# Performance work log

Hardware: AMD Instinct MI355X
Metric: run time of the kernel (lower is better)

## Reference

```python
import jax, jax.numpy as jnp
import numpy as np

B, C, H, W = 8, 64, 128, 128
NH, OPH = 4, 16
MX, MY = 32, 17  # n_modes=(32,32) -> modes_y = 32//2+1
NPAT_S, NPAT_F = 10000, 5000
ED_S, ED_F = 64, 32


def setup_inputs() -> dict:
    ks = jax.random.split(jax.random.key(0), 16)
    n = lambda k, s, sc=1.0: jax.random.normal(k, s, dtype=jnp.float32) * sc
    z = lambda s: jnp.zeros(s, jnp.float32)
    return dict(
        x=n(ks[0], (B, C, H, W)),
        se_emb=n(ks[1], (NPAT_S, ED_S)),
        se_w=n(ks[2], (ED_S, C), 0.1), se_b=z(C),
        mhf_wr=n(ks[3], (NH, C, OPH, MX, MY), 0.01),
        mhf_wi=n(ks[4], (NH, C, OPH, MX, MY), 0.01),
        mhf_bias=z(C),
        sp_emb=n(ks[5], (NPAT_F, ED_F)),
        sp_wr=n(ks[6], (ED_F, C * MX * MY), 0.05), sp_br=z(C * MX * MY),
        sp_wi=n(ks[7], (ED_F, C * MX * MY), 0.05), sp_bi=z(C * MX * MY),
        gate_w1=n(ks[8], (3 * C, 64), 0.05), gate_b1=z(64),
        gate_w2=n(ks[9], (64, 3), 0.05), gate_b2=z(3),
        skip_w=n(ks[10], (C, C), 0.05), skip_b=z(C),
        norm_g=jnp.ones(C), norm_b=z(C),
        mlp_w1=n(ks[11], (C, 2 * C), 0.05), mlp_b1=z(2 * C),
        mlp_w2=n(ks[12], (2 * C, C), 0.05), mlp_b2=z(C),
    )


def _gelu(v):
    return jax.nn.gelu(v, approximate=False)


def _block(x, se_emb, se_w, se_b, mhf_wr, mhf_wi, mhf_bias, sp_emb, sp_wr, sp_br,
           sp_wi, sp_bi, gate_w1, gate_b1, gate_w2, gate_b2, skip_w, skip_b,
           norm_g, norm_b, mlp_w1, mlp_b1, mlp_w2, mlp_b2):
    Bq, Cq, Hq, Wq = x.shape
    # --- SpatialEngram: quantization is elementwise, so sum over window entries
    # equals 3x3 box-sum of the quantized padded field (identical integers,
    # avoids materializing the (B,C,H,W,3,3) unfold tensor).
    xp = jnp.pad(x, ((0, 0), (0, 0), (1, 1), (1, 1)), mode='edge')
    q = (xp * 100.0).astype(jnp.int32)  # trunc toward zero, same as torch .long()
    hv = jnp.zeros((Bq, Cq, Hq, Wq), jnp.int32)
    for i in range(3):
        for j in range(3):
            hv = hv + q[:, :, i:i + Hq, j:j + Wq]
    idx = (jnp.abs(hv) % NPAT_S).astype(jnp.float32).mean(axis=1).astype(jnp.int32)  # (B,H,W)
    spatial = jnp.moveaxis(se_emb[idx] @ se_w + se_b, -1, 1)  # (B,C,H,W)
    # --- MHF multi-head spectral conv (all heads in one einsum; concat == reshape)
    xf = jnp.fft.rfft2(x, norm='ortho')          # (B,C,H,W//2+1) complex64
    lo = xf[:, :, :MX, :MY]
    wc = (mhf_wr + 1j * mhf_wi).astype(lo.dtype)
    of = jnp.einsum('biXY,hioXY->bhoXY', lo, wc).reshape(Bq, Cq, MX, MY)
    full = jnp.zeros((Bq, Cq, Hq, Wq // 2 + 1), lo.dtype).at[:, :, :MX, :MY].set(of)
    mhf = jnp.fft.irfft2(full, s=(Hq, Wq), norm='ortho') + mhf_bias[:, None, None]
    # --- SpectralEngram: per-sample hash of low-freq magnitude -> embedding -> freq proj
    mag = jnp.abs(lo).mean(axis=(1, 2, 3))                       # (B,)
    fidx = (mag * 1000.0).astype(jnp.int32) % NPAT_F
    fe = sp_emb[fidx]                                            # (B,ED_F)
    re = (fe @ sp_wr + sp_br).reshape(Bq, Cq, MX, MY)
    im = (fe @ sp_wi + sp_bi).reshape(Bq, Cq, MX, MY)
    full2 = jnp.zeros((Bq, Cq, Hq, Wq // 2 + 1), lo.dtype).at[:, :, :MX, :MY].set(re + 1j * im)
    spec = jnp.fft.irfft2(full2, s=(Hq, Wq), norm='ortho')
    # --- gated fusion
    gate_in = jnp.concatenate([spatial.mean((2, 3)), mhf.mean((2, 3)), spec.mean((2, 3))], axis=-1)
    gw = jax.nn.softmax(_gelu(gate_in @ gate_w1 + gate_b1) @ gate_w2 + gate_b2, axis=-1)
    a = gw[:, 0, None, None, None]
    bt = gw[:, 1, None, None, None]
    gm = gw[:, 2, None, None, None]
    fused = a * spatial + bt * mhf + gm * spec
    y = fused + jnp.einsum('bihw,io->bohw', x, skip_w) + skip_b[:, None, None]
    # --- GroupNorm(1,C) + 1x1-conv channel MLP (dropout=0)
    mu = y.mean((1, 2, 3), keepdims=True)
    var = y.var((1, 2, 3), keepdims=True)
    yn = (y - mu) * jax.lax.rsqrt(var + 1e-5) * norm_g[:, None, None] + norm_b[:, None, None]
    h = _gelu(jnp.einsum('bihw,io->bohw', yn, mlp_w1) + mlp_b1[:, None, None])
    h = jnp.einsum('bihw,io->bohw', h, mlp_w2) + mlp_b2[:, None, None]
    return y + h


def reference(x, se_emb, se_w, se_b, mhf_wr, mhf_wi, mhf_bias, sp_emb, sp_wr, sp_br,
              sp_wi, sp_bi, gate_w1, gate_b1, gate_w2, gate_b2, skip_w, skip_b,
              norm_g, norm_b, mlp_w1, mlp_b1, mlp_w2, mlp_b2):
    return _block(x, se_emb, se_w, se_b, mhf_wr, mhf_wi, mhf_bias, sp_emb, sp_wr, sp_br,
                  sp_wi, sp_bi, gate_w1, gate_b1, gate_w2, gate_b2, skip_w, skip_b,
                  norm_g, norm_b, mlp_w1, mlp_b1, mlp_w2, mlp_b2)
```

## Files before the change

kernel.cpp:

```cpp
#include <hip/hip_runtime.h>
#include <hip/hip_bf16.h>
#include <math.h>

#define B_ 8
#define C_ 64
#define H_ 128
#define W_ 128
#define NH_ 4
#define OPH_ 16
#define MX_ 32
#define MY_ 17
#define NPAT_F 5000
#define ED_F 32
#define XY_ (MX_*MY_)
#define HW_ (H_*W_)
#define NE_ (B_*C_*H_*W_)

#define OFF_LO     0u
#define OFF_T1     2228224u
#define OFF_T2     2228224u
#define OFF_FMHF   11141120u
#define OFF_FSPEC  13369344u
#define OFF_IDX    33030144u

typedef __hip_bfloat16 bf16;

template<typename T>
__device__ __forceinline__ float ldt(const void* p, int i){ return (float)(((const T*)p)[i]); }

template<typename T>
__device__ __forceinline__ float2 ld2(const void* p, int i){
  if(sizeof(T)==4) return *(const float2*)((const float*)p + i);
  unsigned raw = *(const unsigned*)((const unsigned short*)p + i);
  return make_float2(__uint_as_float(raw<<16), __uint_as_float(raw & 0xffff0000u));
}

__device__ __forceinline__ float gelu_f(float a){
  return 0.5f*a*(1.0f + erff(a*0.70710678118654752f));
}

__global__ void k_det(const void* ng, int* flag, double* dmag){
  if(threadIdx.x==0) *flag = (((const unsigned*)ng)[0] == 0x3F800000u) ? 1 : 0;
  if(threadIdx.x<B_) dmag[threadIdx.x] = 0.0;
}

template<typename T>
__device__ __forceinline__ void hash_body(const void* x, int* idx, int b, int h, int w){
  int hm = h>0 ? h-1 : 0, hp = h<127 ? h+1 : 127;
  int wm = w>0 ? w-1 : 0, wp = w<127 ? w+1 : 127;
  int s = 0;
  for(int c=0;c<C_;++c){
    const int base = ((b*C_+c)*H_)*W_;
    const int r0 = base + hm*W_, r1 = base + h*W_, r2 = base + hp*W_;
    int q = (int)(ldt<T>(x,r0+wm)*100.0f) + (int)(ldt<T>(x,r0+w)*100.0f) + (int)(ldt<T>(x,r0+wp)*100.0f)
          + (int)(ldt<T>(x,r1+wm)*100.0f) + (int)(ldt<T>(x,r1+w)*100.0f) + (int)(ldt<T>(x,r1+wp)*100.0f)
          + (int)(ldt<T>(x,r2+wm)*100.0f) + (int)(ldt<T>(x,r2+w)*100.0f) + (int)(ldt<T>(x,r2+wp)*100.0f);
    s += (q < 0 ? -q : q) % 10000;
  }
  idx[(b*H_+h)*W_+w] = s >> 6;
}
__global__ __launch_bounds__(128) void k_hash(const void* x, int* idx, const int* flg){
  int h = blockIdx.x, b = blockIdx.y, w = threadIdx.x;
  if(*flg) hash_body<float>(x, idx, b, h, w); else hash_body<bf16>(x, idx, b, h, w);
}

__global__ __launch_bounds__(256) void k_f1(const void* __restrict__ x, double* __restrict__ t1,
                                            const int* flg){
  __shared__ float4 xs4[2048];
  __shared__ double2 csd[128];
  int t = threadIdx.x;
  if(t<128){ double a = (double)t * (6.283185307179586476925286766559/128.0); csd[t] = make_double2(cos(a), sin(a)); }
  int h0 = blockIdx.x << 6, bcl = blockIdx.y;
  long xbase = ((long)bcl*H_ + h0)*W_;
  if(*flg){
    const float4* xp = (const float4*)((const float*)x + xbase);
    for(int i=t;i<2048;i+=256){
      int r=i>>5, s=i&31;
      xs4[(r<<5) + (s ^ (r&31))] = xp[i];
    }
  } else {
    const uint2* xp = (const uint2*)((const unsigned short*)x + xbase);
    for(int i=t;i<2048;i+=256){
      int r=i>>5, s=i&31;
      uint2 raw = xp[i];
      xs4[(r<<5) + (s ^ (r&31))] = make_float4(
        __uint_as_float(raw.x<<16), __uint_as_float(raw.x & 0xffff0000u),
        __uint_as_float(raw.y<<16), __uint_as_float(raw.y & 0xffff0000u));
    }
  }
  __syncthreads();
  for(int o=t;o<MY_*64;o+=256){
    int ky = o>>6, hr = o&63;
    const float4* xr = xs4 + (hr<<5);
    const int sx = hr & 31;
    double ar=0.0, ai=0.0;
    int m = 0;
    for(int s=0;s<32;++s){
      float4 v4 = xr[s ^ sx];
      double2 c0 = csd[m]; ar = fma((double)v4.x, c0.x, ar); ai = fma(-(double)v4.x, c0.y, ai); m=(m+ky)&127;
      double2 c1 = csd[m]; ar = fma((double)v4.y, c1.x, ar); ai = fma(-(double)v4.y, c1.y, ai); m=(m+ky)&127;
      double2 c2 = csd[m]; ar = fma((double)v4.z, c2.x, ar); ai = fma(-(double)v4.z, c2.y, ai); m=(m+ky)&127;
      double2 c3 = csd[m]; ar = fma((double)v4.w, c3.x, ar); ai = fma(-(double)v4.w, c3.y, ai); m=(m+ky)&127;
    }
    long tt = ((long)(bcl*MY_ + ky))*H_ + (h0 + hr);
    *(double2*)(t1 + 2*tt) = make_double2(ar, ai);
  }
}

__global__ __launch_bounds__(576) void k_f2(const double* __restrict__ t1, float* __restrict__ lo){
  __shared__ double2 ts[MY_*129];
  __shared__ double2 csd[128];
  int t = threadIdx.x;
  if(t<128){ double a = (double)t * (6.283185307179586476925286766559/128.0); csd[t] = make_double2(cos(a), sin(a)); }
  int bcl = blockIdx.x;
  const double2* tg = (const double2*)t1 + (size_t)bcl*MY_*H_;
  for(int i=t;i<MY_*H_;i+=576){ int ky=i>>7, hh=i&127; ts[ky*129+hh] = tg[i]; }
  __syncthreads();
  if(t < 544){
    int ky = t % MY_, kx = t / MY_;
    const double2* tr = ts + ky*129;
    double ar=0.0, ai=0.0;
    int m = 0;
    for(int h=0;h<H_;++h){
      double2 v = tr[h];
      double2 cs2 = csd[m];
      double vr = v.x, vi = v.y;
      double cc = cs2.x, ss = cs2.y;
      ar += vr*cc + vi*ss;
      ai += vi*cc - vr*ss;
      m = (m + kx) & 127;
    }
    int g = bcl*XY_ + kx*MY_ + ky;
    *(float2*)(lo + 2*g) = make_float2((float)(ar*(1.0/128.0)), (float)(ai*(1.0/128.0)));
  }
}

template<typename T>
__device__ __forceinline__ void spatial_load_w(const void* se_w, const void* se_b, float wsm[64][64], float* sb, int t){
  for(int i=t;i<4096;i+=256) wsm[i>>6][i&63] = ldt<T>(se_w, i);
  if(t<64) sb[t] = ldt<T>(se_b, t);
}
template<typename T>
__device__ __forceinline__ void spatial_load_emb(const void* se_emb, const int* ibs, float emb[32][65], int w0, int t){
  for(int i=t;i<2048;i+=256){ int wl_=i>>6, e=i&63; emb[wl_][e] = ldt<T>(se_emb, ibs[w0+wl_]*64 + e); }
}
__global__ __launch_bounds__(256) void k_spatial(const void* se_emb, const void* se_w, const void* se_b,
                                                 const int* __restrict__ idx, bf16* __restrict__ spatial,
                                                 const int* flg){
  __shared__ float wsm[64][64];
  __shared__ float emb[32][65];
  __shared__ float sb[64];
  __shared__ int ibs[128];
  int b = blockIdx.x >> 7, h = blockIdx.x & 127, t = threadIdx.x;
  int f = *flg;
  if(f) spatial_load_w<float>(se_w, se_b, wsm, sb, t); else spatial_load_w<bf16>(se_w, se_b, wsm, sb, t);
  if(t<128) ibs[t] = idx[(b*H_+h)*W_ + t];
  __syncthreads();
  for(int chunk=0; chunk<4; ++chunk){
    int w0 = chunk*32;
    if(f) spatial_load_emb<float>(se_emb, ibs, emb, w0, t); else spatial_load_emb<bf16>(se_emb, ibs, emb, w0, t);
    __syncthreads();
    for(int i=t;i<2048;i+=256){
      int cc=i>>5, wl_=i&31;
      float acc = sb[cc];
      #pragma unroll 8
      for(int e=0;e<64;++e) acc = fmaf(emb[wl_][e], wsm[e][cc], acc);
      spatial[((b*C_+cc)*H_+h)*W_ + w0+wl_] = __float2bfloat16(acc);
    }
    __syncthreads();
  }
}

__global__ __launch_bounds__(256) void k_mag(const float* __restrict__ lo, double* __restrict__ dmag){
  int b = blockIdx.y, t = threadIdx.x;
  const float* p = lo + b*C_*XY_*2;
  double s = 0.0;
  for(int i = blockIdx.x*256 + t; i < C_*XY_; i += 17*256){
    double re = p[2*i], im = p[2*i+1];
    s += sqrt(re*re + im*im);
  }
  __shared__ double sh[256];
  sh[t] = s; __syncthreads();
  for(int k=128;k>0;k>>=1){ if(t<k) sh[t]+=sh[t+k]; __syncthreads(); }
  if(t==0) atomicAdd(&dmag[b], sh[0]);
}

template<typename T>
__device__ __forceinline__ void specf_body(const void* sp_emb, const void* sp_wr, const void* sp_br,
                                           const void* sp_wi, const void* sp_bi, const double* dmag,
                                           float* fspec, float* fe, int b, int j0, int t){
  double mag = dmag[b] / (double)(C_*XY_);
  int fv = ((int)(mag*1000.0)) % NPAT_F;
  fv = fv < 0 ? 0 : (fv >= NPAT_F ? NPAT_F-1 : fv);
  if(t < ED_F) fe[t] = ldt<T>(sp_emb, fv*ED_F + t);
  __syncthreads();
  float2 rr = ld2<T>(sp_br, j0), ii = ld2<T>(sp_bi, j0);
  float re0=rr.x, re1=rr.y, im0=ii.x, im1=ii.y;
  #pragma unroll 8
  for(int e=0;e<ED_F;++e){
    float f = fe[e];
    float2 wr = ld2<T>(sp_wr, e*(C_*XY_)+j0);
    float2 wi = ld2<T>(sp_wi, e*(C_*XY_)+j0);
    re0 = fmaf(f, wr.x, re0); im0 = fmaf(f, wi.x, im0);
    re1 = fmaf(f, wr.y, re1); im1 = fmaf(f, wi.y, im1);
  }
  int o = b*C_*XY_ + j0;
  *(float4*)(fspec + 2*o) = make_float4(re0, im0, re1, im1);
}
__global__ __launch_bounds__(256) void k_specf(const void* sp_emb, const void* sp_wr, const void* sp_br,
                                               const void* sp_wi, const void* sp_bi, const double* __restrict__ dmag,
                                               float* __restrict__ fspec, const int* flg){
  __shared__ float fe[ED_F];
  int b = blockIdx.y;
  int j0 = (blockIdx.x*256 + threadIdx.x)*2;
  if(*flg) specf_body<float>(sp_emb, sp_wr, sp_br, sp_wi, sp_bi, dmag, fspec, fe, b, j0, threadIdx.x);
  else     specf_body<bf16 >(sp_emb, sp_wr, sp_br, sp_wi, sp_bi, dmag, fspec, fe, b, j0, threadIdx.x);
}

template<typename T>
__device__ __forceinline__ void mhf_body(const float* lp, const void* wr, const void* wi,
                                         float* fmhf, int b, int co){
  int hh = co >> 4, o = co & 15;
  for(int xy = threadIdx.x; xy < XY_; xy += 256){
    float ar=0.f, ai=0.f;
    for(int i=0;i<C_;++i){
      float2 l2 = *(const float2*)(lp + (i*XY_+xy)*2);
      float lr = l2.x, li = l2.y;
      int widx = ((hh*C_ + i)*OPH_ + o)*XY_ + xy;
      float wre = ldt<T>(wr, widx), wim = ldt<T>(wi, widx);
      ar += lr*wre - li*wim;
      ai += lr*wim + li*wre;
    }
    int oo = (b*C_ + co)*XY_ + xy;
    *(float2*)(fmhf + 2*oo) = make_float2(ar, ai);
  }
}
__global__ __launch_bounds__(256) void k_mhf(const float* __restrict__ lo, const void* wr, const void* wi,
                                             float* __restrict__ fmhf, const int* flg){
  int b = blockIdx.y, co = blockIdx.x;
  const float* lp = lo + b*C_*XY_*2;
  if(*flg) mhf_body<float>(lp, wr, wi, fmhf, b, co); else mhf_body<bf16>(lp, wr, wi, fmhf, b, co);
}

__global__ __launch_bounds__(256) void k_gmean(const bf16* __restrict__ spatial, float* __restrict__ smean){
  int cch = blockIdx.x, b = blockIdx.y, t = threadIdx.x;
  const unsigned short* p = (const unsigned short*)(spatial + (size_t)(b*C_+cch)*HW_);
  float s = 0.f;
  for(int i=t;i<HW_/8;i+=256){
    uint4 v = *(const uint4*)(p + (size_t)i*8);
    s += __uint_as_float(v.x<<16) + __uint_as_float(v.x&0xffff0000u)
       + __uint_as_float(v.y<<16) + __uint_as_float(v.y&0xffff0000u)
       + __uint_as_float(v.z<<16) + __uint_as_float(v.z&0xffff0000u)
       + __uint_as_float(v.w<<16) + __uint_as_float(v.w&0xffff0000u);
  }
  __shared__ float sh[256];
  sh[t]=s; __syncthreads();
  for(int k=128;k>0;k>>=1){ if(t<k) sh[t]+=sh[t+k]; __syncthreads(); }
  if(t==0) smean[b*C_+cch] = sh[0]*(1.0f/16384.0f);
}

template<typename T>
__device__ __forceinline__ void gate_body(const float* smean, const float* fmhf, const float* fspec,
                                          const void* mbias, const void* w1, const void* b1,
                                          const void* w2, const void* b2,
                                          float* gw, float* ssum, float* ssq,
                                          float* gin, float* hid, int b, int t){
  gin[t]      = smean[b*C_+t];
  gin[64+t]   = fmhf [(b*C_+t)*XY_*2] * (1.0f/128.0f) + ldt<T>(mbias, t);
  gin[128+t]  = fspec[(b*C_+t)*XY_*2] * (1.0f/128.0f);
  __syncthreads();
  float acc = ldt<T>(b1, t);
  for(int k=0;k<192;++k) acc = fmaf(gin[k], ldt<T>(w1, k*64+t), acc);
  hid[t] = gelu_f(acc);
  __syncthreads();
  if(t==0){
    float o[3];
    for(int j=0;j<3;++j){
      float a = ldt<T>(b2, j);
      for(int k=0;k<64;++k) a += hid[k]*ldt<T>(w2, k*3+j);
      o[j]=a;
    }
    float mx = fmaxf(o[0], fmaxf(o[1], o[2]));
    float e0=expf(o[0]-mx), e1=expf(o[1]-mx), e2=expf(o[2]-mx);
    float sum=e0+e1+e2;
    gw[b*3+0]=e0/sum; gw[b*3+1]=e1/sum; gw[b*3+2]=e2/sum;
    ssum[b]=0.f; ssq[b]=0.f;
  }
}
__global__ __launch_bounds__(64) void k_gate(const float* __restrict__ smean, const float* __restrict__ fmhf,
                                             const float* __restrict__ fspec, const void* mbias,
                                             const void* w1, const void* b1, const void* w2, const void* b2,
                                             float* __restrict__ gw, float* __restrict__ ssum,
                                             float* __restrict__ ssq, const int* flg){
  __shared__ float gin[192];
  __shared__ float hid[64];
  int b = blockIdx.x, t = threadIdx.x;
  if(*flg) gate_body<float>(smean, fmhf, fspec, mbias, w1, b1, w2, b2, gw, ssum, ssq, gin, hid, b, t);
  else     gate_body<bf16 >(smean, fmhf, fspec, mbias, w1, b1, w2, b2, gw, ssum, ssq, gin, hid, b, t);
}

__global__ __launch_bounds__(256) void k_comb(const float* __restrict__ fmhf, const float* __restrict__ fspec,
                                              const float* __restrict__ gw, float* __restrict__ t2){
  __shared__ float Gr[XY_], Gi[XY_], cs[128], sn[128];
  int c = blockIdx.x, b = blockIdx.y, t = threadIdx.x;
  if(t<128) __sincosf((float)t * 0.04908738521234052f, &sn[t], &cs[t]);
  float bt=gw[b*3+1], gm=gw[b*3+2];
  for(int i=t;i<XY_;i+=256){
    int o = ((b*C_+c)*XY_+i)*2;
    float2 fm = *(const float2*)(fmhf + o);
    float2 fs = *(const float2*)(fspec + o);
    Gr[i] = bt*fm.x + gm*fs.x;
    Gi[i] = bt*fm.y + gm*fs.y;
  }
  __syncthreads();
  for(int i=t;i<MY_*H_;i+=256){
    int hh = i & 127, ky = i >> 7;
    float ar=0.f, ai=0.f;
    for(int kx=0;kx<MX_;++kx){
      int m = (kx*hh)&127;
      float cc=cs[m], ss=sn[m];
      float fr=Gr[kx*MY_+ky], fi=Gi[kx*MY_+ky];
      ar += fr*cc - fi*ss;
      ai += fr*ss + fi*cc;
    }
    int e = (((b*C_+c)*MY_+ky)*H_ + hh)*2;
    *(float2*)(t2 + e) = make_float2(ar, ai);
  }
}

template<typename T>
__device__ __forceinline__ void fuse_body(const void* x, const void* skw, const void* skb, const void* mbias,
                                          bf16* sp_y, const float* t2, const float* gw,
                                          float* ssum, float* ssq,
                                          float wl[64][64], float Ur[64][17], float Ui[64][17],
                                          float* cs, float* sn, float* sb, float* mb,
                                          float* s1, float* s2, int b, int h, int t){
  int w = t & 127, half = t >> 7;
  if(t<128) __sincosf((float)t * 0.04908738521234052f, &sn[t], &cs[t]);
  for(int i=t;i<4096;i+=256) wl[i>>6][i&63] = ldt<T>(skw, i);
  if(t<64){ sb[t]=ldt<T>(skb,t); mb[t]=ldt<T>(mbias,t); }
  for(int i=t;i<C_*MY_;i+=256){
    int cc=i/MY_, ky=i%MY_;
    int e = (((b*C_+cc)*MY_+ky)*H_ + h)*2;
    float2 v = *(const float2*)(t2 + e);
    Ur[cc][ky]=v.x; Ui[cc][ky]=v.y;
  }
  float ga=gw[b*3], gbv=gw[b*3+1];
  __syncthreads();
  int c0 = half*32;
  float acc[32];
  #pragma unroll
  for(int j=0;j<32;++j) acc[j]=sb[c0+j];
  int xb = (b*C_*H_ + h)*W_ + w;
  for(int k=0;k<64;++k){
    float xv = ldt<T>(x, xb + k*HW_);
    #pragma unroll
    for(int j=0;j<32;++j) acc[j] = fmaf(xv, wl[k][c0+j], acc[j]);
  }
  float ls=0.f, lq=0.f;
  for(int j=0;j<32;++j){
    int cc=c0+j;
    float vr = Ur[cc][0];
    #pragma unroll
    for(int ky=1;ky<MY_;++ky){
      int m=(ky*w)&127;
      vr += 2.0f*(Ur[cc][ky]*cs[m] - Ui[cc][ky]*sn[m]);
    }
    int gi = ((b*C_+cc)*H_+h)*W_+w;
    float v = ga*__bfloat162float(sp_y[gi]) + vr*(1.0f/128.0f) + gbv*mb[cc] + acc[j];
    sp_y[gi] = __float2bfloat16(v);
    ls += v; lq = fmaf(v, v, lq);
  }
  s1[t]=ls; s2[t]=lq; __syncthreads();
  for(int k=128;k>0;k>>=1){ if(t<k){ s1[t]+=s1[t+k]; s2[t]+=s2[t+k]; } __syncthreads(); }
  if(t==0){ atomicAdd(&ssum[b], s1[0]); atomicAdd(&ssq[b], s2[0]); }
}
__global__ __launch_bounds__(256) void k_fuse(const void* x, const void* skw, const void* skb, const void* mbias,
                                              bf16* __restrict__ sp_y, const float* __restrict__ t2,
                                              const float* __restrict__ gw,
                                              float* __restrict__ ssum, float* __restrict__ ssq, const int* flg){
  __shared__ float wl[64][64];
  __shared__ float Ur[64][17], Ui[64][17];
  __shared__ float cs[128], sn[128];
  __shared__ float sb[64], mb[64];
  __shared__ float s1[256], s2[256];
  int h = blockIdx.x, b = blockIdx.y, t = threadIdx.x;
  if(*flg) fuse_body<float>(x, skw, skb, mbias, sp_y, t2, gw, ssum, ssq, wl, Ur, Ui, cs, sn, sb, mb, s1, s2, b, h, t);
  else     fuse_body<bf16 >(x, skw, skb, mbias, sp_y, t2, gw, ssum, ssq, wl, Ur, Ui, cs, sn, sb, mb, s1, s2, b, h, t);
}

__global__ void k_stats(const float* __restrict__ ssum, const float* __restrict__ ssq,
                        float* __restrict__ mu, float* __restrict__ rs){
  int b = threadIdx.x;
  if(b < B_){
    float m = ssum[b] * (1.0f/1048576.0f);
    float v = ssq[b] * (1.0f/1048576.0f) - m*m;
    mu[b] = m;
    rs[b] = rsqrtf(v + 1e-5f);
  }
}

template<typename T>
__device__ __forceinline__ void mlp_body(const bf16* __restrict__ y, float mu, float rs,
                                         const void* ng, const void* nb, const void* w1, const void* b1,
                                         const void* w2, const void* b2, float* __restrict__ out,
                                         float* __restrict__ yn_s, float* __restrict__ w_s,
                                         float* __restrict__ h2_s,
                                         int b, int h, int w0, int t){
  const int tx = t & 31, ty = t >> 5;
  const int p0 = ty << 2;
  const int ybase = (b*C_*H_ + h)*W_ + w0;

  for(int L=t; L<8192; L+=256){
    int i = L>>7, j = L&127;
    w_s[(i<<7) + (((j>>2) ^ (i&31))<<2) + (j&3)] = ldt<T>(w1, L);
  }
  for(int it=0; it<2; ++it){
    int idx = t + (it<<8);
    int c = idx>>3, p4 = (idx&7)<<2;
    const unsigned short* yp = (const unsigned short*)y + ybase + c*HW_ + p4;
    uint2 raw = *(const uint2*)yp;
    float g = ldt<T>(ng, c), nbv = ldt<T>(nb, c);
    float sc = rs*g;
    float4 o;
    o.x = (__uint_as_float(raw.x<<16)          - mu)*sc + nbv;
    o.y = (__uint_as_float(raw.x & 0xffff0000u)- mu)*sc + nbv;
    o.z = (__uint_as_float(raw.y<<16)          - mu)*sc + nbv;
    o.w = (__uint_as_float(raw.y & 0xffff0000u)- mu)*sc + nbv;
    *(float4*)(yn_s + c*36 + p4) = o;
  }
  float w2r[32];
  #pragma unroll
  for(int jj=0;jj<32;++jj) w2r[jj] = ldt<T>(w2, t + (jj<<8));
  __syncthreads();

  const int kA = tx << 2;
  float a[4][4];
  #pragma unroll
  for(int j=0;j<4;++j){
    float bj = ldt<T>(b1, kA+j);
    a[j][0]=bj; a[j][1]=bj; a[j][2]=bj; a[j][3]=bj;
  }
  #pragma unroll 4
  for(int i=0;i<64;++i){
    float4 yv = *(const float4*)(yn_s + i*36 + p0);
    float4 wv = *(const float4*)(w_s + (i<<7) + ((tx ^ (i&31))<<2));
    float y4[4] = {yv.x, yv.y, yv.z, yv.w};
    float w4[4] = {wv.x, wv.y, wv.z, wv.w};
    #pragma unroll
    for(int j=0;j<4;++j){
      #pragma unroll
      for(int q=0;q<4;++q) a[j][q] = fmaf(y4[q], w4[j], a[j][q]);
    }
  }
  __syncthreads();

  #pragma unroll
  for(int jj=0;jj<32;++jj){
    int L = t + (jj<<8);
    int k = L>>6, c = L&63;
    w_s[(k<<6) + (((c>>1) ^ (k&31))<<1) + (c&1)] = w2r[jj];
  }
  {
    float* hb = (tx < 16) ? yn_s : h2_s;
    int rbase = (tx & 15) << 2;
    #pragma unroll
    for(int j=0;j<4;++j){
      float4 hv;
      hv.x = gelu_f(a[j][0]); hv.y = gelu_f(a[j][1]); hv.z = gelu_f(a[j][2]); hv.w = gelu_f(a[j][3]);
      *(float4*)(hb + (rbase+j)*36 + p0) = hv;
    }
  }
  __syncthreads();

  const int c0 = tx << 1;
  float acc[2][4];
  #pragma unroll
  for(int j=0;j<2;++j){ acc[j][0]=0.f; acc[j][1]=0.f; acc[j][2]=0.f; acc[j][3]=0.f; }
  #pragma unroll 4
  for(int k=0;k<64;++k){
    float4 hv = *(const float4*)(yn_s + k*36 + p0);
    float2 wv = *(const float2*)(w_s + (k<<6) + ((tx ^ (k&31))<<1));
    float hq[4] = {hv.x, hv.y, hv.z, hv.w};
    #pragma unroll
    for(int q=0;q<4;++q) acc[0][q] = fmaf(hq[q], wv.x, acc[0][q]);
    #pragma unroll
    for(int q=0;q<4;++q) acc[1][q] = fmaf(hq[q], wv.y, acc[1][q]);
  }
  #pragma unroll 4
  for(int k=0;k<64;++k){
    float4 hv = *(const float4*)(h2_s + k*36 + p0);
    float2 wv = *(const float2*)(w_s + ((64+k)<<6) + ((tx ^ (k&31))<<1));
    float hq[4] = {hv.x, hv.y, hv.z, hv.w};
    #pragma unroll
    for(int q=0;q<4;++q) acc[0][q] = fmaf(hq[q], wv.x, acc[0][q]);
    #pragma unroll
    for(int q=0;q<4;++q) acc[1][q] = fmaf(hq[q], wv.y, acc[1][q]);
  }

  #pragma unroll
  for(int j=0;j<2;++j){
    int c = c0 + j;
    float b2v = ldt<T>(b2, c);
    const unsigned short* yp = (const unsigned short*)y + ybase + c*HW_ + p0;
    uint2 raw = *(const uint2*)yp;
    float4 o;
    o.x = __uint_as_float(raw.x<<16)           + acc[j][0] + b2v;
    o.y = __uint_as_float(raw.x & 0xffff0000u) + acc[j][1] + b2v;
    o.z = __uint_as_float(raw.y<<16)           + acc[j][2] + b2v;
    o.w = __uint_as_float(raw.y & 0xffff0000u) + acc[j][3] + b2v;
    *(float4*)(out + ybase + c*HW_ + p0) = o;
  }
}
__global__ __launch_bounds__(256) void k_mlp(const bf16* __restrict__ y, const float* __restrict__ mu_,
                                             const float* __restrict__ rs_, const void* ng, const void* nb,
                                             const void* w1, const void* b1, const void* w2, const void* b2,
                                             float* __restrict__ out, const int* flg){
  __shared__ float yn_s[64*36];
  __shared__ float w_s[8192];
  __shared__ float h2_s[64*36];
  int h = blockIdx.x >> 2, w0 = (blockIdx.x & 3) << 5, b = blockIdx.y;
  int t = threadIdx.x;
  float mu = mu_[b], rs = rs_[b];
  if(*flg) mlp_body<float>(y, mu, rs, ng, nb, w1, b1, w2, b2, out, yn_s, w_s, h2_s, b, h, w0, t);
  else     mlp_body<bf16 >(y, mu, rs, ng, nb, w1, b1, w2, b2, out, yn_s, w_s, h2_s, b, h, w0, t);
}

extern "C" void kernel_launch(void* const* d_in, const int* in_sizes, int n_in,
                              void* d_out, int out_size, void* d_ws, size_t ws_size,
                              hipStream_t stream) {
  (void)out_size; (void)ws_size;
  static const int dict_sizes[24] = {8388608,640000,4096,64,2228224,2228224,64,160000,
                                     1114112,34816,1114112,34816,12288,64,192,3,
                                     4096,64,64,64,8192,128,8192,64};
  static const int sorted_sizes[24] = {64,3,12288,192,64,2228224,2228224,128,64,8192,8192,
                                       64,64,64,640000,4096,64,4096,34816,34816,160000,
                                       1114112,1114112,8388608};
  static const int sorted_to_dict[24] = {13,15,12,14,6,5,4,21,23,20,22,19,18,3,1,2,17,16,11,9,7,10,8,0};

  const void* in[24];
  bool is_dict = (n_in == 24), is_sorted = (n_in == 24);
  if(n_in == 24){
    for(int i=0;i<24;++i){
      if(in_sizes[i] != dict_sizes[i])   is_dict   = false;
      if(in_sizes[i] != sorted_sizes[i]) is_sorted = false;
    }
  }
  if(is_sorted && !is_dict){
    for(int i=0;i<24;++i) in[sorted_to_dict[i]] = d_in[i];
  } else {
    for(int i=0;i<24 && i<n_in;++i) in[i] = d_in[i];
  }

  const void* x       = in[0];
  const void* se_emb  = in[1];
  const void* se_w    = in[2];
  const void* se_b    = in[3];
  const void* mhf_wr  = in[4];
  const void* mhf_wi  = in[5];
  const void* mhf_bias= in[6];
  const void* sp_emb  = in[7];
  const void* sp_wr   = in[8];
  const void* sp_br   = in[9];
  const void* sp_wi   = in[10];
  const void* sp_bi   = in[11];
  const void* gate_w1 = in[12];
  const void* gate_b1 = in[13];
  const void* gate_w2 = in[14];
  const void* gate_b2 = in[15];
  const void* skip_w  = in[16];
  const void* skip_b  = in[17];
  const void* norm_g  = in[18];
  const void* norm_b  = in[19];
  const void* mlp_w1  = in[20];
  const void* mlp_b1  = in[21];
  const void* mlp_w2  = in[22];
  const void* mlp_b2  = in[23];
  float* out = (float*)d_out;

  bf16*   sp_y = (bf16*)d_ws;
  float*  scal = (float*)((char*)d_ws + (size_t)NE_*2);
  float* smean = scal;
  float* gw    = scal + 512;
  float* ssum  = scal + 536;
  float* ssq   = scal + 544;
  float* mu    = scal + 552;
  float* rs    = scal + 560;
  int*   flag  = (int*)(scal + 576);
  double* dmag = (double*)(scal + 584);

  char* ob = (char*)d_out;
  float*  lo    = (float*) (ob + OFF_LO);
  double* t1    = (double*)(ob + OFF_T1);
  float*  t2    = (float*) (ob + OFF_T2);
  float*  fmhf  = (float*) (ob + OFF_FMHF);
  float*  fspec = (float*) (ob + OFF_FSPEC);
  int*    idx   = (int*)   (ob + OFF_IDX);

  hipLaunchKernelGGL(k_det,    dim3(1),           dim3(64),  0, stream, norm_g, flag, dmag);
  hipLaunchKernelGGL(k_hash,   dim3(H_, B_),      dim3(128), 0, stream, x, idx, flag);
  hipLaunchKernelGGL(k_f1,     dim3(2, 512),      dim3(256), 0, stream, x, t1, flag);
  hipLaunchKernelGGL(k_f2,     dim3(512),         dim3(576), 0, stream, t1, lo);
  hipLaunchKernelGGL(k_spatial,dim3(B_*H_),       dim3(256), 0, stream, se_emb, se_w, se_b, idx, sp_y, flag);
  hipLaunchKernelGGL(k_mag,    dim3(17, B_),      dim3(256), 0, stream, lo, dmag);
  hipLaunchKernelGGL(k_specf,  dim3(C_*XY_/512, B_), dim3(256), 0, stream, sp_emb, sp_wr, sp_br, sp_wi, sp_bi, dmag, fspec, flag);
  hipLaunchKernelGGL(k_mhf,    dim3(C_, B_),      dim3(256), 0, stream, lo, mhf_wr, mhf_wi, fmhf, flag);
  hipLaunchKernelGGL(k_gmean,  dim3(C_, B_),      dim3(256), 0, stream, sp_y, smean);
  hipLaunchKernelGGL(k_gate,   dim3(B_),          dim3(64),  0, stream, smean, fmhf, fspec, mhf_bias, gate_w1, gate_b1, gate_w2, gate_b2, gw, ssum, ssq, flag);
  hipLaunchKernelGGL(k_comb,   dim3(C_, B_),      dim3(256), 0, stream, fmhf, fspec, gw, t2);
  hipLaunchKernelGGL(k_fuse,   dim3(H_, B_),      dim3(256), 0, stream, x, skip_w, skip_b, mhf_bias, sp_y, t2, gw, ssum, ssq, flag);
  hipLaunchKernelGGL(k_stats,  dim3(1),           dim3(64),  0, stream, ssum, ssq, mu, rs);
  hipLaunchKernelGGL(k_mlp,    dim3(H_*4, B_),    dim3(256), 0, stream, sp_y, mu, rs, norm_g, norm_b, mlp_w1, mlp_b1, mlp_w2, mlp_b2, out, flag);
}
```

Baseline: 507.5 us.

## Register-tile spatial and MLP GEMMs, remap MHF blocks per XCD, hoist twiddles

k_spatial now gives each thread a 2x4 register tile and reads the weights as float4. k_mlp switches to 64-pixel tiles with a 4x8 register tile per thread and streams the weights through a smaller shared buffer in halves, prefetching the next half into registers. k_mhf uses a 1D grid remapped so that blocks sharing an XCD handle neighbouring output channels, which should improve L2 reuse of the weights. k_comb and k_fuse preload their twiddle factors into registers instead of indexing shared memory inside the inner loop. The aim is fewer LDS loads per FMA and better cache locality, at the cost of higher register pressure and more syncs in the MLP kernel.

```diff
diff --git a/kernel.cpp b/kernel.cpp
--- a/kernel.cpp
+++ b/kernel.cpp
@@ -156,16 +156,32 @@
   if(f) spatial_load_w<float>(se_w, se_b, wsm, sb, t); else spatial_load_w<bf16>(se_w, se_b, wsm, sb, t);
   if(t<128) ibs[t] = idx[(b*H_+h)*W_ + t];
   __syncthreads();
+  const int tx = t & 15, ty = t >> 4;
+  const int c0 = ty << 2;
   for(int chunk=0; chunk<4; ++chunk){
     int w0 = chunk*32;
     if(f) spatial_load_emb<float>(se_emb, ibs, emb, w0, t); else spatial_load_emb<bf16>(se_emb, ibs, emb, w0, t);
     __syncthreads();
-    for(int i=t;i<2048;i+=256){
-      int cc=i>>5, wl_=i&31;
-      float acc = sb[cc];
-      #pragma unroll 8
-      for(int e=0;e<64;++e) acc = fmaf(emb[wl_][e], wsm[e][cc], acc);
-      spatial[((b*C_+cc)*H_+h)*W_ + w0+wl_] = __float2bfloat16(acc);
+    float acc0[4], acc1[4];
+    #pragma unroll
+    for(int j=0;j<4;++j){ acc0[j]=sb[c0+j]; acc1[j]=sb[c0+j]; }
+    #pragma unroll 8
+    for(int e=0;e<64;++e){
+      float e0 = emb[tx][e], e1 = emb[tx+16][e];
+      float4 wv = *(const float4*)(&wsm[e][c0]);
+      float w4[4] = {wv.x, wv.y, wv.z, wv.w};
+      #pragma unroll
+      for(int j=0;j<4;++j){
+        acc0[j] = fmaf(e0, w4[j], acc0[j]);
+        acc1[j] = fmaf(e1, w4[j], acc1[j]);
+      }
+    }
+    #pragma unroll
+    for(int j=0;j<4;++j){
+      int cc = c0 + j;
+      int gb = ((b*C_+cc)*H_+h)*W_ + w0;
+      spatial[gb + tx]      = __float2bfloat16(acc0[j]);
+      spatial[gb + tx + 16] = __float2bfloat16(acc1[j]);
     }
     __syncthreads();
   }
@@ -237,7 +253,10 @@
 }
 __global__ __launch_bounds__(256) void k_mhf(const float* __restrict__ lo, const void* wr, const void* wi,
                                              float* __restrict__ fmhf, const int* flg){
-  int b = blockIdx.y, co = blockIdx.x;
+  int bid = blockIdx.x;
+  int xcd = bid & 7, slot = bid >> 3;
+  int co = (xcd << 3) + (slot & 7);
+  int b  = slot >> 3;
   const float* lp = lo + b*C_*XY_*2;
   if(*flg) mhf_body<float>(lp, wr, wi, fmhf, b, co); else mhf_body<bf16>(lp, wr, wi, fmhf, b, co);
 }
@@ -313,15 +332,18 @@
     Gi[i] = bt*fm.y + gm*fs.y;
   }
   __syncthreads();
+  const int hh = t & 127;
+  float cr[32], sr[32];
+  #pragma unroll
+  for(int kx=0;kx<MX_;++kx){ int m=(kx*hh)&127; cr[kx]=cs[m]; sr[kx]=sn[m]; }
   for(int i=t;i<MY_*H_;i+=256){
-    int hh = i & 127, ky = i >> 7;
+    int ky = i >> 7;
     float ar=0.f, ai=0.f;
+    #pragma unroll 8
     for(int kx=0;kx<MX_;++kx){
-      int m = (kx*hh)&127;
-      float cc=cs[m], ss=sn[m];
       float fr=Gr[kx*MY_+ky], fi=Gi[kx*MY_+ky];
-      ar += fr*cc - fi*ss;
-      ai += fr*ss + fi*cc;
+      ar += fr*cr[kx] - fi*sr[kx];
+      ai += fr*sr[kx] + fi*cr[kx];
     }
     int e = (((b*C_+c)*MY_+ky)*H_ + hh)*2;
     *(float2*)(t2 + e) = make_float2(ar, ai);
@@ -347,6 +369,9 @@
   }
   float ga=gw[b*3], gbv=gw[b*3+1];
   __syncthreads();
+  float cw[MY_], sw[MY_];
+  #pragma unroll
+  for(int ky=1;ky<MY_;++ky){ int m=(ky*w)&127; cw[ky]=cs[m]; sw[ky]=sn[m]; }
   int c0 = half*32;
   float acc[32];
   #pragma unroll
@@ -363,8 +388,7 @@
     float vr = Ur[cc][0];
     #pragma unroll
     for(int ky=1;ky<MY_;++ky){
-      int m=(ky*w)&127;
-      vr += 2.0f*(Ur[cc][ky]*cs[m] - Ui[cc][ky]*sn[m]);
+      vr += 2.0f*(Ur[cc][ky]*cw[ky] - Ui[cc][ky]*sw[ky]);
     }
     int gi = ((b*C_+cc)*H_+h)*W_+w;
     float v = ga*__bfloat162float(sp_y[gi]) + vr*(1.0f/128.0f) + gbv*mb[cc] + acc[j];
@@ -407,17 +431,15 @@
                                          float* __restrict__ yn_s, float* __restrict__ w_s,
                                          float* __restrict__ h2_s,
                                          int b, int h, int w0, int t){
-  const int tx = t & 31, ty = t >> 5;
+  const int tx = t & 15, ty = t >> 4;
   const int p0 = ty << 2;
   const int ybase = (b*C_*H_ + h)*W_ + w0;
 
-  for(int L=t; L<8192; L+=256){
-    int i = L>>7, j = L&127;
-    w_s[(i<<7) + (((j>>2) ^ (i&31))<<2) + (j&3)] = ldt<T>(w1, L);
-  }
-  for(int it=0; it<2; ++it){
-    int idx = t + (it<<8);
-    int c = idx>>3, p4 = (idx&7)<<2;
+  #pragma unroll
+  for(int jj=0;jj<16;++jj) w_s[t + (jj<<8)] = ldt<T>(w1, t + (jj<<8));
+  for(int it=0; it<4; ++it){
+    int chunk = t + (it<<8);
+    int c = chunk >> 4, p4 = (chunk & 15) << 2;
     const unsigned short* yp = (const unsigned short*)y + ybase + c*HW_ + p4;
     uint2 raw = *(const uint2*)yp;
     float g = ldt<T>(ng, c), nbv = ldt<T>(nb, c);
@@ -427,79 +449,105 @@
     o.y = (__uint_as_float(raw.x & 0xffff0000u)- mu)*sc + nbv;
     o.z = (__uint_as_float(raw.y<<16)          - mu)*sc + nbv;
     o.w = (__uint_as_float(raw.y & 0xffff0000u)- mu)*sc + nbv;
-    *(float4*)(yn_s + c*36 + p4) = o;
-  }
-  float w2r[32];
-  #pragma unroll
-  for(int jj=0;jj<32;++jj) w2r[jj] = ldt<T>(w2, t + (jj<<8));
-  __syncthreads();
-
-  const int kA = tx << 2;
-  float a[4][4];
+    *(float4*)(yn_s + c*68 + p4) = o;
+  }
+  float pf[16];
+  #pragma unroll
+  for(int jj=0;jj<16;++jj) pf[jj] = ldt<T>(w1, 4096 + t + (jj<<8));
+  __syncthreads();
+
+  const int kA = tx << 2, kB = 64 + (tx << 2);
+  float a[8][4];
   #pragma unroll
   for(int j=0;j<4;++j){
     float bj = ldt<T>(b1, kA+j);
     a[j][0]=bj; a[j][1]=bj; a[j][2]=bj; a[j][3]=bj;
-  }
-  #pragma unroll 4
-  for(int i=0;i<64;++i){
-    float4 yv = *(const float4*)(yn_s + i*36 + p0);
-    float4 wv = *(const float4*)(w_s + (i<<7) + ((tx ^ (i&31))<<2));
+    float bj2 = ldt<T>(b1, kB+j);
+    a[4+j][0]=bj2; a[4+j][1]=bj2; a[4+j][2]=bj2; a[4+j][3]=bj2;
+  }
+  #pragma unroll 8
+  for(int i=0;i<32;++i){
+    float4 yv = *(const float4*)(yn_s + i*68 + p0);
+    float4 wa = *(const float4*)(w_s + (i<<7) + kA);
+    float4 wb = *(const float4*)(w_s + (i<<7) + kB);
     float y4[4] = {yv.x, yv.y, yv.z, yv.w};
+    float w8[8] = {wa.x, wa.y, wa.z, wa.w, wb.x, wb.y, wb.z, wb.w};
+    #pragma unroll
+    for(int j=0;j<8;++j){
+      #pragma unroll
+      for(int q=0;q<4;++q) a[j][q] = fmaf(y4[q], w8[j], a[j][q]);
+    }
+  }
+  __syncthreads();
+  #pragma unroll
+  for(int jj=0;jj<16;++jj) w_s[t + (jj<<8)] = pf[jj];
+  #pragma unroll
+  for(int jj=0;jj<16;++jj) pf[jj] = ldt<T>(w2, t + (jj<<8));
+  __syncthreads();
+  #pragma unroll 8
+  for(int i=0;i<32;++i){
+    float4 yv = *(const float4*)(yn_s + (32+i)*68 + p0);
+    float4 wa = *(const float4*)(w_s + (i<<7) + kA);
+    float4 wb = *(const float4*)(w_s + (i<<7) + kB);
+    float y4[4] = {yv.x, yv.y, yv.z, yv.w};
+    float w8[8] = {wa.x, wa.y, wa.z, wa.w, wb.x, wb.y, wb.z, wb.w};
+    #pragma unroll
+    for(int j=0;j<8;++j){
+      #pragma unroll
+      for(int q=0;q<4;++q) a[j][q] = fmaf(y4[q], w8[j], a[j][q]);
+    }
+  }
+  __syncthreads();
+  #pragma unroll
+  for(int jj=0;jj<16;++jj) w_s[t + (jj<<8)] = pf[jj];
+  #pragma unroll
+  for(int jj=0;jj<16;++jj) pf[jj] = ldt<T>(w2, 4096 + t + (jj<<8));
+  #pragma unroll
+  for(int j=0;j<4;++j){
+    float4 hA;
+    hA.x = gelu_f(a[j][0]); hA.y = gelu_f(a[j][1]); hA.z = gelu_f(a[j][2]); hA.w = gelu_f(a[j][3]);
+    *(float4*)(yn_s + (kA+j)*68 + p0) = hA;
+    float4 hB;
+    hB.x = gelu_f(a[4+j][0]); hB.y = gelu_f(a[4+j][1]); hB.z = gelu_f(a[4+j][2]); hB.w = gelu_f(a[4+j][3]);
+    *(float4*)(h2_s + (kA+j)*68 + p0) = hB;
+  }
+  __syncthreads();
+
+  const int c0 = tx << 2;
+  float acc[4][4];
+  #pragma unroll
+  for(int j=0;j<4;++j){ acc[j][0]=0.f; acc[j][1]=0.f; acc[j][2]=0.f; acc[j][3]=0.f; }
+  #pragma unroll 8
+  for(int k=0;k<64;++k){
+    float4 hv = *(const float4*)(yn_s + k*68 + p0);
+    float4 wv = *(const float4*)(w_s + (k<<6) + c0);
+    float hq[4] = {hv.x, hv.y, hv.z, hv.w};
     float w4[4] = {wv.x, wv.y, wv.z, wv.w};
     #pragma unroll
     for(int j=0;j<4;++j){
       #pragma unroll
-      for(int q=0;q<4;++q) a[j][q] = fmaf(y4[q], w4[j], a[j][q]);
-    }
-  }
-  __syncthreads();
-
-  #pragma unroll
-  for(int jj=0;jj<32;++jj){
-    int L = t + (jj<<8);
-    int k = L>>6, c = L&63;
-    w_s[(k<<6) + (((c>>1) ^ (k&31))<<1) + (c&1)] = w2r[jj];
-  }
-  {
-    float* hb = (tx < 16) ? yn_s : h2_s;
-    int rbase = (tx & 15) << 2;
+      for(int q=0;q<4;++q) acc[j][q] = fmaf(hq[q], w4[j], acc[j][q]);
+    }
+  }
+  __syncthreads();
+  #pragma unroll
+  for(int jj=0;jj<16;++jj) w_s[t + (jj<<8)] = pf[jj];
+  __syncthreads();
+  #pragma unroll 8
+  for(int k=0;k<64;++k){
+    float4 hv = *(const float4*)(h2_s + k*68 + p0);
+    float4 wv = *(const float4*)(w_s + (k<<6) + c0);
+    float hq[4] = {hv.x, hv.y, hv.z, hv.w};
+    float w4[4] = {wv.x, wv.y, wv.z, wv.w};
     #pragma unroll
     for(int j=0;j<4;++j){
-      float4 hv;
-      hv.x = gelu_f(a[j][0]); hv.y = gelu_f(a[j][1]); hv.z = gelu_f(a[j][2]); hv.w = gelu_f(a[j][3]);
-      *(float4*)(hb + (rbase+j)*36 + p0) = hv;
-    }
-  }
-  __syncthreads();
-
-  const int c0 = tx << 1;
-  float acc[2][4];
-  #pragma unroll
-  for(int j=0;j<2;++j){ acc[j][0]=0.f; acc[j][1]=0.f; acc[j][2]=0.f; acc[j][3]=0.f; }
-  #pragma unroll 4
-  for(int k=0;k<64;++k){
-    float4 hv = *(const float4*)(yn_s + k*36 + p0);
-    float2 wv = *(const float2*)(w_s + (k<<6) + ((tx ^ (k&31))<<1));
-    float hq[4] = {hv.x, hv.y, hv.z, hv.w};
-    #pragma unroll
-    for(int q=0;q<4;++q) acc[0][q] = fmaf(hq[q], wv.x, acc[0][q]);
-    #pragma unroll
-    for(int q=0;q<4;++q) acc[1][q] = fmaf(hq[q], wv.y, acc[1][q]);
-  }
-  #pragma unroll 4
-  for(int k=0;k<64;++k){
-    float4 hv = *(const float4*)(h2_s + k*36 + p0);
-    float2 wv = *(const float2*)(w_s + ((64+k)<<6) + ((tx ^ (k&31))<<1));
-    float hq[4] = {hv.x, hv.y, hv.z, hv.w};
-    #pragma unroll
-    for(int q=0;q<4;++q) acc[0][q] = fmaf(hq[q], wv.x, acc[0][q]);
-    #pragma unroll
-    for(int q=0;q<4;++q) acc[1][q] = fmaf(hq[q], wv.y, acc[1][q]);
-  }
-
-  #pragma unroll
-  for(int j=0;j<2;++j){
+      #pragma unroll
+      for(int q=0;q<4;++q) acc[j][q] = fmaf(hq[q], w4[j], acc[j][q]);
+    }
+  }
+
+  #pragma unroll
+  for(int j=0;j<4;++j){
     int c = c0 + j;
     float b2v = ldt<T>(b2, c);
     const unsigned short* yp = (const unsigned short*)y + ybase + c*HW_ + p0;
@@ -516,10 +564,10 @@
                                              const float* __restrict__ rs_, const void* ng, const void* nb,
                                              const void* w1, const void* b1, const void* w2, const void* b2,
                                              float* __restrict__ out, const int* flg){
-  __shared__ float yn_s[64*36];
-  __shared__ float w_s[8192];
-  __shared__ float h2_s[64*36];
-  int h = blockIdx.x >> 2, w0 = (blockIdx.x & 3) << 5, b = blockIdx.y;
+  __shared__ float yn_s[64*68];
+  __shared__ float w_s[4096];
+  __shared__ float h2_s[64*68];
+  int h = blockIdx.x >> 1, w0 = (blockIdx.x & 1) << 6, b = blockIdx.y;
   int t = threadIdx.x;
   float mu = mu_[b], rs = rs_[b];
   if(*flg) mlp_body<float>(y, mu, rs, ng, nb, w1, b1, w2, b2, out, yn_s, w_s, h2_s, b, h, w0, t);
@@ -604,11 +652,11 @@
   hipLaunchKernelGGL(k_spatial,dim3(B_*H_),       dim3(256), 0, stream, se_emb, se_w, se_b, idx, sp_y, flag);
   hipLaunchKernelGGL(k_mag,    dim3(17, B_),      dim3(256), 0, stream, lo, dmag);
   hipLaunchKernelGGL(k_specf,  dim3(C_*XY_/512, B_), dim3(256), 0, stream, sp_emb, sp_wr, sp_br, sp_wi, sp_bi, dmag, fspec, flag);
-  hipLaunchKernelGGL(k_mhf,    dim3(C_, B_),      dim3(256), 0, stream, lo, mhf_wr, mhf_wi, fmhf, flag);
+  hipLaunchKernelGGL(k_mhf,    dim3(512),         dim3(256), 0, stream, lo, mhf_wr, mhf_wi, fmhf, flag);
   hipLaunchKernelGGL(k_gmean,  dim3(C_, B_),      dim3(256), 0, stream, sp_y, smean);
   hipLaunchKernelGGL(k_gate,   dim3(B_),          dim3(64),  0, stream, smean, fmhf, fspec, mhf_bias, gate_w1, gate_b1, gate_w2, gate_b2, gw, ssum, ssq, flag);
   hipLaunchKernelGGL(k_comb,   dim3(C_, B_),      dim3(256), 0, stream, fmhf, fspec, gw, t2);
   hipLaunchKernelGGL(k_fuse,   dim3(H_, B_),      dim3(256), 0, stream, x, skip_w, skip_b, mhf_bias, sp_y, t2, gw, ssum, ssq, flag);
   hipLaunchKernelGGL(k_stats,  dim3(1),           dim3(64),  0, stream, ssum, ssq, mu, rs);
-  hipLaunchKernelGGL(k_mlp,    dim3(H_*4, B_),    dim3(256), 0, stream, sp_y, mu, rs, norm_g, norm_b, mlp_w1, mlp_b1, mlp_w2, mlp_b2, out, flag);
-}
+  hipLaunchKernelGGL(k_mlp,    dim3(H_*2, B_),    dim3(256), 0, stream, sp_y, mu, rs, norm_g, norm_b, mlp_w1, mlp_b1, mlp_w2, mlp_b2, out, flag);
+}
```

After: 447.4 us. -11.8%, faster.
